# Kernel tuning notes

Measured on AMD Instinct MI355X. Metric: run time of the kernel, lower is better.

Reference implementation:

```python
import jax, jax.numpy as jnp
import numpy as np


def conv2d(x, w, groups=1, pad=0):
    # x: [N,C,H,W], w: [O, C//groups, kh, kw]
    return jax.lax.conv_general_dilated(
        x, w, window_strides=(1, 1), padding=[(pad, pad), (pad, pad)],
        dimension_numbers=("NCHW", "OIHW", "NCHW"), feature_group_count=groups)


def l2norm(x, eps=1e-12):
    # torch F.normalize over last dim: x / max(||x||_2, eps)
    n = jnp.sqrt(jnp.sum(x * x, axis=-1, keepdims=True))
    return x / jnp.maximum(n, eps)


def setup_inputs() -> dict:
    key = jax.random.key(0)
    dim, heads, b, H, W = 48, 8, 2, 256, 256
    ks = jax.random.split(key, 20)
    rn = lambda k, shp, s: (jax.random.normal(k, shp, dtype=jnp.float32) * s)
    return {
        "x1": rn(ks[0], (b, dim, H, W), 1.0),
        "x2": rn(ks[1], (b, dim, H, W), 1.0),
        "t1": jnp.ones((heads, 1, 1), jnp.float32),
        "t2": jnp.ones((heads, 1, 1), jnp.float32),
        "qkv1_w": rn(ks[2], (dim * 3, dim, 1, 1), 0.05),
        "qkv1_dw": rn(ks[3], (dim * 3, 1, 3, 3), 0.05),
        "qkv2_w": rn(ks[4], (dim * 3, dim, 1, 1), 0.05),
        "qkv2_dw": rn(ks[5], (dim * 3, 1, 3, 3), 0.05),
        "mid1_w": rn(ks[6], (dim, dim, 1, 1), 0.05),
        "mid2_w": rn(ks[7], (dim, dim, 1, 1), 0.05),
        "pE_w": rn(ks[8], (dim * 8, dim * 2, 1, 1), 0.05),
        "pE_dw": rn(ks[9], (dim * 8, 1, 3, 3), 0.05),
        "pE1_w": rn(ks[10], (dim * 4, dim, 1, 1), 0.05),
        "pE1_dw": rn(ks[11], (dim * 4, 1, 3, 3), 0.05),
        "pE2_w": rn(ks[12], (dim * 4, dim, 1, 1), 0.05),
        "pE2_dw": rn(ks[13], (dim * 4, 1, 3, 3), 0.05),
        "po1_w": rn(ks[14], (dim * 2, dim * 4, 1, 1), 0.05),
        "po2_w": rn(ks[15], (dim * 2, dim * 4, 1, 1), 0.05),
    }


def reference(x1, x2, t1, t2, qkv1_w, qkv1_dw, qkv2_w, qkv2_dw,
              mid1_w, mid2_w, pE_w, pE_dw, pE1_w, pE1_dw,
              pE2_w, pE2_dw, po1_w, po2_w):
    b, c, h, w = x1.shape
    heads = t1.shape[0]
    ch = c // heads  # channels per head

    def to_heads(t):  # [b, c, h, w] -> [b, heads, ch, h*w]
        return t.reshape(b, heads, ch, h * w)

    qkv1 = conv2d(conv2d(x1, qkv1_w), qkv1_dw, groups=3 * c, pad=1)
    q1, k1, v1 = jnp.split(qkv1, 3, axis=1)
    qkv2 = conv2d(conv2d(x2, qkv2_w), qkv2_dw, groups=3 * c, pad=1)
    q2, k2, v2 = jnp.split(qkv2, 3, axis=1)

    q1, k1, v1 = to_heads(q1), to_heads(k1), to_heads(v1)
    q2, k2, v2 = to_heads(q2), to_heads(k2), to_heads(v2)
    q1, k1 = l2norm(q1), l2norm(k1)
    q2, k2 = l2norm(q2), l2norm(k2)

    # channel cross-attention: [b, heads, ch, ch]
    attn1 = jnp.einsum("bhcn,bhdn->bhcd", q2, k1) * t1
    attn2 = jnp.einsum("bhcn,bhdn->bhcd", q1, k2) * t2
    out1 = jnp.einsum("bhcd,bhdn->bhcn", jax.nn.softmax(attn1, axis=-1), v1)
    out2 = jnp.einsum("bhcd,bhdn->bhcn", jax.nn.softmax(attn2, axis=-1), v2)
    out1 = out1.reshape(b, c, h, w)
    out2 = out2.reshape(b, c, h, w)

    x1 = x1 + conv2d(out1, mid1_w)
    x2 = x2 + conv2d(out2, mid2_w)
    out = jnp.concatenate([x1, x2], axis=1)  # [b, 2c, h, w]

    g = conv2d(conv2d(out, pE_w), pE_dw, groups=8 * c, pad=1)  # [b, 8c, h, w]
    g1, g2 = jnp.split(g, 2, axis=1)
    x1 = jax.nn.gelu(g1, approximate=False) * conv2d(conv2d(x1, pE1_w), pE1_dw, groups=4 * c, pad=1)
    x2 = jax.nn.gelu(g2, approximate=False) * conv2d(conv2d(x2, pE2_w), pE2_dw, groups=4 * c, pad=1)

    return out + conv2d(x1, po1_w) + conv2d(x2, po2_w)
```

## Files before the change

### kernel.cpp

```cpp
#include <hip/hip_runtime.h>
#include <math.h>

#define HW_ 65536

typedef __attribute__((ext_vector_type(8))) short b16x8;
typedef __attribute__((ext_vector_type(4))) short b16x4;
typedef __attribute__((ext_vector_type(4))) float f32x4;
typedef __attribute__((ext_vector_type(2))) float f32x2;

__device__ __forceinline__ unsigned short f2b(float f) {
    union { float f; unsigned u; } v; v.f = f;
    unsigned r = v.u + 0x7fffu + ((v.u >> 16) & 1u);
    return (unsigned short)(r >> 16);
}
__device__ __forceinline__ float b2f(unsigned short h) {
    union { unsigned u; float f; } v; v.u = ((unsigned)h) << 16; return v.f;
}
__device__ __forceinline__ float gelu_f(float x) {
    float t = 0.7978845608f * fmaf(0.044715f * x, x * x, x);
    float e = __expf(2.f * t);
    float th = 1.f - 2.f / (e + 1.f);
    return 0.5f * x * (1.f + th);
}

__device__ __forceinline__ f32x2 pk_fma(f32x2 a, f32x2 b, f32x2 c) {
#if __has_builtin(__builtin_elementwise_fma)
    return __builtin_elementwise_fma(a, b, c);
#else
    f32x2 r; r[0] = fmaf(a[0], b[0], c[0]); r[1] = fmaf(a[1], b[1], c[1]);
    return r;
#endif
}

__device__ __forceinline__ float wave_reduce_sum(float v) {
    #pragma unroll
    for (int off = 32; off; off >>= 1) v += __shfl_down(v, off, 64);
    return v;
}

__device__ __forceinline__ size_t baddr(long px, int CC, int g) {
    return (((size_t)(px >> 4)) * CC + g) * 128 + ((size_t)(px & 15) << 3);
}

__global__ __launch_bounds__(256) void wprep_k(
    const float* __restrict__ q1w, const float* __restrict__ q2w,
    const float* __restrict__ m1w, const float* __restrict__ m2w,
    const float* __restrict__ pEw, const float* __restrict__ p1w,
    const float* __restrict__ p2w, const float* __restrict__ o1w,
    const float* __restrict__ o2w,
    const float* __restrict__ q1dw, const float* __restrict__ q2dw,
    const float* __restrict__ pEdw, const float* __restrict__ p1dw,
    const float* __restrict__ p2dw,
    unsigned short* __restrict__ wt, float* __restrict__ dwt)
{
    const int idx = blockIdx.x * 256 + threadIdx.x;
    if (idx < 135168) {
        const int base[8] = {0,9216,18432,21504,24576,61440,98304,116736};
        int s = 0;
        #pragma unroll
        for (int i = 1; i < 8; i++) if (idx >= base[i]) s = i;
        const int local = idx - base[s];
        float v = 0.f;
        if (s < 4) {
            const int m = local >> 6, k = local & 63;
            const float* src = (s == 0) ? q1w : (s == 1) ? q2w : (s == 2) ? m1w : m2w;
            if (k < 48) v = src[m * 48 + k];
        } else if (s < 6) {
            const int br = s - 4;
            const int m = local / 96, k = local % 96;
            if (m < 192) {
                v = pEw[(size_t)(br * 192 + m) * 96 + k];
            } else {
                const float* p12 = br ? p2w : p1w;
                const int lo = br * 48, m2 = m - 192;
                if (k >= lo && k < lo + 48) v = p12[m2 * 48 + (k - lo)];
            }
        } else {
            const int m = local / 192, k = local % 192;
            v = ((s == 6) ? o1w : o2w)[m * 192 + k];
        }
        wt[idx] = f2b(v);
    } else if (idx < 135168 + 9504) {
        const int d = idx - 135168;
        const int dbase[5] = {0,1296,2592,6048,7776};
        const int Cs[5] = {144,144,384,192,192};
        int s = 0;
        #pragma unroll
        for (int i = 1; i < 5; i++) if (d >= dbase[i]) s = i;
        const int local = d - dbase[s], C = Cs[s];
        const int t = local / C, c = local % C;
        const float* src = (s == 0) ? q1dw : (s == 1) ? q2dw : (s == 2) ? pEdw
                         : (s == 3) ? p1dw : p2dw;
        dwt[d] = src[c * 9 + t];
    }
}

template<int BM, int KC, int NT, int BSRC, int EPI, int GRIDMODE>
__global__ __launch_bounds__(256) void gemm_k(
    const unsigned short* __restrict__ B16,
    const float* __restrict__ Bf32, int Cin,
    const unsigned short* __restrict__ W16,
    unsigned short* __restrict__ out16, int CCo, int Coff,
    float* __restrict__ outf, const unsigned short* __restrict__ res,
    const unsigned short* __restrict__ acc16,
    const float* __restrict__ Bf32b, const unsigned short* __restrict__ W16b,
    unsigned short* __restrict__ out16b)
{
    constexpr int MF = BM / 16;
    const int tid = threadIdx.x;
    const int lane = tid & 63, w = tid >> 6;
    const int lm = lane & 15, lk = lane >> 4;

    int mb, pxblk;
    if (GRIDMODE == 2) {
        const int bx = blockIdx.x;
        const int sb = (bx & 7) * 512 + (bx >> 3);
        mb = sb & 3; pxblk = sb >> 2;
    } else {
        mb = blockIdx.y; pxblk = blockIdx.x;
    }

    const float* Bf = Bf32;
    const unsigned short* Wp = W16;
    unsigned short* outp = out16;
    if (GRIDMODE == 0 && BSRC == 1 && blockIdx.z) {
        Bf = Bf32b; Wp = W16b; outp = out16b;
    }

    const int m0 = mb * BM;
    const long wavepx = ((long)pxblk * 4 + w) * (NT * 16);
    const long pxb0 = wavepx >> 4;

    f32x4 acc[NT][MF];
    #pragma unroll
    for (int nt = 0; nt < NT; nt++)
        #pragma unroll
        for (int m = 0; m < MF; m++)
            #pragma unroll
            for (int j = 0; j < 4; j++) acc[nt][m][j] = 0.f;

    #pragma unroll
    for (int kc = 0; kc < KC; kc++) {
        b16x8 a[MF];
        #pragma unroll
        for (int m = 0; m < MF; m++)
            a[m] = *(const b16x8*)&Wp[(size_t)(m0 + m * 16 + lm) * (KC * 32) + kc * 32 + lk * 8];
        #pragma unroll
        for (int nt = 0; nt < NT; nt++) {
            b16x8 bb;
            if (BSRC == 0) {
                bb = *(const b16x8*)&B16[((pxb0 + nt) * (KC * 4) + (kc * 4 + lk)) * 128 + lm * 8];
            } else {
                const long px = wavepx + nt * 16 + lm;
                const int p = (int)(px & 65535), bat = (int)(px >> 16);
                #pragma unroll
                for (int j = 0; j < 8; j++) {
                    const int c = kc * 32 + lk * 8 + j;
                    float v = (c < Cin) ? Bf[((size_t)(bat * Cin + c) << 16) + p] : 0.f;
                    bb[j] = (short)f2b(v);
                }
            }
            #pragma unroll
            for (int m = 0; m < MF; m++)
                acc[nt][m] = __builtin_amdgcn_mfma_f32_16x16x32_bf16(a[m], bb, acc[nt][m], 0, 0, 0);
        }
    }

    #pragma unroll
    for (int nt = 0; nt < NT; nt++) {
        const long px = wavepx + nt * 16 + lm;
        #pragma unroll
        for (int m = 0; m < MF; m++) {
            const int mrow = m * 16 + lk * 4;
            if (EPI == 0) {
                b16x4 o;
                #pragma unroll
                for (int j = 0; j < 4; j++) o[j] = (short)f2b(acc[nt][m][j]);
                const int ch = Coff + m0 + mrow;
                *(b16x4*)&outp[((pxb0 + nt) * CCo + (ch >> 3)) * 128 + lm * 8 + (ch & 7)] = o;
            } else if (EPI == 1) {
                const int p = (int)(px & 65535), bat = (int)(px >> 16);
                b16x4 r4 = *(const b16x4*)&res[((pxb0 + nt) * 12 + (mrow >> 3)) * 128 + lm * 8 + (mrow & 7)];
                #pragma unroll
                for (int j = 0; j < 4; j++)
                    outf[((size_t)(bat * 96 + mrow + j) << 16) + p]
                        = acc[nt][m][j] + b2f((unsigned short)r4[j]);
            } else if (EPI == 2) {
                const int p = (int)(px & 65535), bat = (int)(px >> 16);
                #pragma unroll
                for (int j = 0; j < 4; j++) {
                    const size_t adr = ((size_t)(bat * 96 + mrow + j) << 16) + p;
                    outf[adr] += acc[nt][m][j];
                }
            } else {
                const int p = (int)(px & 65535), bat = (int)(px >> 16);
                const size_t boffi = ((pxb0 + nt) * 12 + (mrow >> 3)) * 128 + lm * 8 + (mrow & 7);
                b16x4 r4 = *(const b16x4*)&res[boffi];
                b16x4 a4 = *(const b16x4*)&acc16[boffi];
                #pragma unroll
                for (int j = 0; j < 4; j++)
                    outf[((size_t)(bat * 96 + mrow + j) << 16) + p]
                        = acc[nt][m][j] + b2f((unsigned short)r4[j]) + b2f((unsigned short)a4[j]);
            }
        }
    }
}

__device__ __forceinline__ void unpack8v(const uint4 u, f32x2 f[4]) {
    union { unsigned u; float f; } a, b;
    a.u = u.x << 16; b.u = u.x & 0xFFFF0000u; f[0][0] = a.f; f[0][1] = b.f;
    a.u = u.y << 16; b.u = u.y & 0xFFFF0000u; f[1][0] = a.f; f[1][1] = b.f;
    a.u = u.z << 16; b.u = u.z & 0xFFFF0000u; f[2][0] = a.f; f[2][1] = b.f;
    a.u = u.w << 16; b.u = u.w & 0xFFFF0000u; f[3][0] = a.f; f[3][1] = b.f;
}

__device__ __forceinline__ void dw_row4(
    f32x2 acc[4][4], const unsigned short* __restrict__ T,
    size_t cb, long lOff, long rOff, bool lval, bool rval,
    const float* __restrict__ wrow, int wstr)
{
    f32x2 w[3][4];
    #pragma unroll
    for (int tx = 0; tx < 3; tx++) {
        const float4 a = *(const float4*)(wrow + (size_t)tx * wstr);
        const float4 b = *(const float4*)(wrow + (size_t)tx * wstr + 4);
        w[tx][0][0] = a.x; w[tx][0][1] = a.y;
        w[tx][1][0] = a.z; w[tx][1][1] = a.w;
        w[tx][2][0] = b.x; w[tx][2][1] = b.y;
        w[tx][3][0] = b.z; w[tx][3][1] = b.w;
    }
    uint4 u[6];
    if (lval) u[0] = *(const uint4*)&T[cb + lOff];
    else      u[0] = make_uint4(0u, 0u, 0u, 0u);
    #pragma unroll
    for (int c = 0; c < 4; c++) u[c + 1] = *(const uint4*)&T[cb + (size_t)c * 8];
    if (rval) u[5] = *(const uint4*)&T[cb + rOff];
    else      u[5] = make_uint4(0u, 0u, 0u, 0u);

    #pragma unroll
    for (int d = 0; d < 6; d++) {
        f32x2 f[4];
        unpack8v(u[d], f);
        #pragma unroll
        for (int tx = 0; tx < 3; tx++) {
            const int p = d - tx;
            if (p >= 0 && p < 4)
                #pragma unroll
                for (int q = 0; q < 4; q++)
                    acc[p][q] = pk_fma(w[tx][q], f[q], acc[p][q]);
        }
    }
}

__device__ __forceinline__ void dw_row2(
    f32x2 acc[2][4], const unsigned short* __restrict__ T,
    size_t cb, long lOff, long rOff, bool lval, bool rval,
    const float* __restrict__ wrow, int wstr)
{
    f32x2 w[3][4];
    #pragma unroll
    for (int tx = 0; tx < 3; tx++) {
        const float4 a = *(const float4*)(wrow + (size_t)tx * wstr);
        const float4 b = *(const float4*)(wrow + (size_t)tx * wstr + 4);
        w[tx][0][0] = a.x; w[tx][0][1] = a.y;
        w[tx][1][0] = a.z; w[tx][1][1] = a.w;
        w[tx][2][0] = b.x; w[tx][2][1] = b.y;
        w[tx][3][0] = b.z; w[tx][3][1] = b.w;
    }
    uint4 u[4];
    if (lval) u[0] = *(const uint4*)&T[cb + lOff];
    else      u[0] = make_uint4(0u, 0u, 0u, 0u);
    u[1] = *(const uint4*)&T[cb];
    u[2] = *(const uint4*)&T[cb + 8];
    if (rval) u[3] = *(const uint4*)&T[cb + rOff];
    else      u[3] = make_uint4(0u, 0u, 0u, 0u);

    #pragma unroll
    for (int c = 0; c < 4; c++) {
        f32x2 f[4];
        unpack8v(u[c], f);
        #pragma unroll
        for (int tx = 0; tx < 3; tx++) {
            const int p = c - tx;
            if (p >= 0 && p < 2)
                #pragma unroll
                for (int q = 0; q < 4; q++)
                    acc[p][q] = pk_fma(w[tx][q], f[q], acc[p][q]);
        }
    }
}

__global__ __launch_bounds__(256) void dw144_k(
    const unsigned short* __restrict__ in1, unsigned short* __restrict__ out1,
    const unsigned short* __restrict__ in2, unsigned short* __restrict__ out2,
    const float* __restrict__ dwt)
{
    const int z = blockIdx.z;
    const unsigned short* in = z ? in2 : in1;
    unsigned short* out = z ? out2 : out1;
    const float* wt = dwt + z * 1296;
    const int bx = blockIdx.x;
    const int sb = (bx & 7) * 288 + (bx >> 3);
    const int idx = sb * 256 + threadIdx.x;
    const int pbi = idx / 72;
    const int rem = idx - pbi * 72;
    const int g = rem >> 2, i = rem & 3;
    const long px0 = (long)pbi * 16 + i * 4;
    const int x0 = (int)(px0 & 255);
    const int y = (int)((px0 >> 8) & 255);
    const bool lval = x0 > 0, rval = x0 < 252;
    const int off = (int)(px0 & 15) * 8;
    const size_t cb0 = ((size_t)(px0 >> 4) * 18 + g) * 128 + off;
    const long lOff = (off == 0) ? (120 - 18 * 128) : -8;
    const long rOff = (off == 96) ? (18 * 128 - 96) : 32;
    const long dyStep = 16 * 18 * 128;

    f32x2 acc[4][4];
    #pragma unroll
    for (int p = 0; p < 4; p++)
        #pragma unroll
        for (int q = 0; q < 4; q++) { acc[p][q][0] = 0.f; acc[p][q][1] = 0.f; }

    #pragma unroll
    for (int dy = -1; dy <= 1; dy++) {
        const int yy = y + dy;
        if ((unsigned)yy >= 256u) continue;
        const size_t cb = cb0 + (size_t)((long)dy * dyStep);
        dw_row4(acc, in, cb, lOff, rOff, lval, rval,
                wt + g * 8 + (size_t)(dy + 1) * 3 * 144, 144);
    }

    #pragma unroll
    for (int p = 0; p < 4; p++) {
        b16x8 o;
        #pragma unroll
        for (int j = 0; j < 8; j++) o[j] = (short)f2b(acc[p][j >> 1][j & 1]);
        *(b16x8*)&out[cb0 + (size_t)p * 8] = o;
    }
}

__global__ __launch_bounds__(256) void dwtail_k(
    const unsigned short* __restrict__ GH, unsigned short* __restrict__ Xg,
    const float* __restrict__ dwtG, const float* __restrict__ dwtH)
{
    const int bx = blockIdx.x;
    const int sb = (bx & 7) * 768 + (bx >> 3);
    const int idx = sb * 256 + threadIdx.x;
    const int pbi = idx / 192;
    const int rem = idx - pbi * 192;
    const int g = rem >> 3, i = rem & 7;
    const long px0 = (long)pbi * 16 + i * 2;
    const int x0 = (int)(px0 & 255);
    const int y = (int)((px0 >> 8) & 255);
    const bool lval = x0 > 0, rval = x0 < 254;
    const int off = (int)(px0 & 15) * 8;
    const size_t cb0 = ((size_t)(px0 >> 4) * 48 + g) * 128 + off;
    const long lOff = (off == 0) ? (120 - 48 * 128) : -8;
    const long rOff = (off == 112) ? (48 * 128 - 112) : 16;
    const long dyStep = 16 * 48 * 128;

    f32x2 aG[2][4], aH[2][4];
    #pragma unroll
    for (int p = 0; p < 2; p++)
        #pragma unroll
        for (int q = 0; q < 4; q++) {
            aG[p][q][0] = 0.f; aG[p][q][1] = 0.f;
            aH[p][q][0] = 0.f; aH[p][q][1] = 0.f;
        }

    #pragma unroll
    for (int dy = -1; dy <= 1; dy++) {
        const int yy = y + dy;
        if ((unsigned)yy >= 256u) continue;
        const size_t cb = cb0 + (size_t)((long)dy * dyStep);
        dw_row2(aG, GH, cb, lOff, rOff, lval, rval,
                dwtG + g * 8 + (size_t)(dy + 1) * 3 * 384, 384);
        dw_row2(aH, GH, cb + 3072, lOff, rOff, lval, rval,
                dwtH + g * 8 + (size_t)(dy + 1) * 3 * 192, 192);
    }

    const size_t ob = ((size_t)(px0 >> 4) * 24 + g) * 128 + off;
    #pragma unroll
    for (int p = 0; p < 2; p++) {
        b16x8 o;
        #pragma unroll
        for (int j = 0; j < 8; j++)
            o[j] = (short)f2b(gelu_f(aG[p][j >> 1][j & 1]) * aH[p][j >> 1][j & 1]);
        *(b16x8*)&Xg[ob + (size_t)p * 8] = o;
    }
}

__global__ __launch_bounds__(256) void attnA_k(
    const unsigned short* __restrict__ Q1, const unsigned short* __restrict__ Q2,
    float* __restrict__ part)
{
    const int tid = threadIdx.x;
    const int chunk = blockIdx.x, bh = blockIdx.y, a = blockIdx.z;
    const int b = bh >> 3, h = bh & 7;
    const unsigned* Qq = (const unsigned*)(a ? Q1 : Q2);
    const unsigned* Qk = (const unsigned*)(a ? Q2 : Q1);
    const int u0 = h * 3;
    const int cq = u0 >> 2, o = u0 & 3;
    const int ck = (24 + u0) >> 2;

    float dot[36], nq[6], nk[6];
    #pragma unroll
    for (int i = 0; i < 36; i++) dot[i] = 0.f;
    #pragma unroll
    for (int i = 0; i < 6; i++) { nq[i] = 0.f; nk[i] = 0.f; }

    #pragma unroll 1
    for (int r = 0; r < 8; r++) {
        const long px = (long)b * 65536 + chunk * 2048 + r * 256 + tid;
        const size_t rowu = ((size_t)(px >> 4)) * 18 * 64 + ((px & 15) << 2);
        const uint4 qa = *(const uint4*)&Qq[rowu + (size_t)cq * 64];
        const uint4 qb = *(const uint4*)&Qq[rowu + (size_t)(cq + 1) * 64];
        const uint4 ka = *(const uint4*)&Qk[rowu + (size_t)ck * 64];
        const uint4 kb = *(const uint4*)&Qk[rowu + (size_t)(ck + 1) * 64];
        unsigned uq[3], uk[3];
        if (o == 0)      { uq[0]=qa.x; uq[1]=qa.y; uq[2]=qa.z; uk[0]=ka.x; uk[1]=ka.y; uk[2]=ka.z; }
        else if (o == 1) { uq[0]=qa.y; uq[1]=qa.z; uq[2]=qa.w; uk[0]=ka.y; uk[1]=ka.z; uk[2]=ka.w; }
        else if (o == 2) { uq[0]=qa.z; uq[1]=qa.w; uq[2]=qb.x; uk[0]=ka.z; uk[1]=ka.w; uk[2]=kb.x; }
        else             { uq[0]=qa.w; uq[1]=qb.x; uq[2]=qb.y; uk[0]=ka.w; uk[1]=kb.x; uk[2]=kb.y; }
        float q[6], k[6];
        #pragma unroll
        for (int i = 0; i < 3; i++) {
            union { unsigned u; float f; } lo, hi;
            lo.u = uq[i] << 16; hi.u = uq[i] & 0xFFFF0000u;
            q[2 * i] = lo.f; q[2 * i + 1] = hi.f;
            lo.u = uk[i] << 16; hi.u = uk[i] & 0xFFFF0000u;
            k[2 * i] = lo.f; k[2 * i + 1] = hi.f;
        }
        #pragma unroll
        for (int c = 0; c < 6; c++) nq[c] = fmaf(q[c], q[c], nq[c]);
        #pragma unroll
        for (int d = 0; d < 6; d++) nk[d] = fmaf(k[d], k[d], nk[d]);
        #pragma unroll
        for (int c = 0; c < 6; c++)
            #pragma unroll
            for (int d = 0; d < 6; d++) dot[c * 6 + d] = fmaf(q[c], k[d], dot[c * 6 + d]);
    }

    __shared__ float red[4][48];
    const int lane = tid & 63, wid = tid >> 6;
    #pragma unroll
    for (int i = 0; i < 48; i++) {
        float v = (i < 36) ? dot[i] : (i < 42 ? nq[i - 36] : nk[i - 42]);
        v = wave_reduce_sum(v);
        if (!lane) red[wid][i] = v;
    }
    __syncthreads();
    if (tid < 48)
        part[((size_t)((a * 16 + bh) * 32 + chunk)) * 48 + tid]
            = red[0][tid] + red[1][tid] + red[2][tid] + red[3][tid];
}

__global__ void attnB_k(const float* __restrict__ part,
                        const float* __restrict__ t1, const float* __restrict__ t2,
                        float* __restrict__ att)
{
    const int abh = blockIdx.x, tid = threadIdx.x;
    const int a = abh >> 4, b = (abh >> 3) & 1, h = abh & 7;
    __shared__ float s[48];
    if (tid < 48) {
        float v = 0.f;
        for (int ch = 0; ch < 32; ch++) v += part[((size_t)abh * 32 + ch) * 48 + tid];
        s[tid] = v;
    }
    __syncthreads();
    if (tid < 6) {
        const int c = tid;
        const float tv = a ? t2[h] : t1[h];
        const float qn = fmaxf(sqrtf(s[36 + c]), 1e-12f);
        float raw[6];
        #pragma unroll
        for (int d = 0; d < 6; d++)
            raw[d] = tv * s[c * 6 + d] / (qn * fmaxf(sqrtf(s[42 + d]), 1e-12f));
        float m = raw[0];
        #pragma unroll
        for (int d = 1; d < 6; d++) m = fmaxf(m, raw[d]);
        float e[6], sum = 0.f;
        #pragma unroll
        for (int d = 0; d < 6; d++) { e[d] = expf(raw[d] - m); sum += e[d]; }
        const float inv = 1.f / sum;
        #pragma unroll
        for (int d = 0; d < 6; d++)
            att[((size_t)(a * 2 + b) * 8 + h) * 36 + c * 6 + d] = e[d] * inv;
    }
}

__global__ __launch_bounds__(256) void mid_k(
    const unsigned short* __restrict__ Q1, const unsigned short* __restrict__ Q2,
    const float* __restrict__ att,
    const float* __restrict__ x1, const float* __restrict__ x2,
    const unsigned short* __restrict__ Wm, unsigned short* __restrict__ D16p)
{
    const int br = blockIdx.y;
    const unsigned short* Qv = br ? Q2 : Q1;
    const float* x = br ? x2 : x1;
    const unsigned short* W16 = Wm + br * 3072;
    const float* attb = att + br * 576;
    const int boff = br * 48;

    __shared__ float atts[288];
    __shared__ unsigned short S[256][72];
    const int tid = threadIdx.x;
    const long px = (long)blockIdx.x * 256 + tid;
    const int bat = (int)(px >> 16);

    for (int i = tid; i < 288; i += 256) atts[i] = attb[bat * 288 + i];

    float v[48];
    #pragma unroll
    for (int i = 0; i < 6; i++) {
        b16x8 t = *(const b16x8*)&Qv[baddr(px, 18, 12 + i)];
        #pragma unroll
        for (int j = 0; j < 8; j++) v[i * 8 + j] = b2f((unsigned short)t[j]);
    }
    __syncthreads();

    #pragma unroll
    for (int h = 0; h < 8; h++) {
        unsigned short sh[6];
        #pragma unroll
        for (int c = 0; c < 6; c++) {
            float s = 0.f;
            #pragma unroll
            for (int d = 0; d < 6; d++) s = fmaf(atts[h * 36 + c * 6 + d], v[h * 6 + d], s);
            sh[c] = f2b(s);
        }
        #pragma unroll
        for (int i = 0; i < 3; i++) {
            unsigned packed = (unsigned)sh[2 * i] | ((unsigned)sh[2 * i + 1] << 16);
            *(unsigned*)&S[tid][h * 6 + 2 * i] = packed;
        }
    }
    #pragma unroll
    for (int i = 0; i < 8; i++) *(unsigned*)&S[tid][48 + 2 * i] = 0u;
    __syncthreads();

    const int lane = tid & 63, w = tid >> 6;
    const int lm = lane & 15, lk = lane >> 4;
    f32x4 acc[4][3];
    #pragma unroll
    for (int nt = 0; nt < 4; nt++)
        #pragma unroll
        for (int m = 0; m < 3; m++)
            #pragma unroll
            for (int j = 0; j < 4; j++) acc[nt][m][j] = 0.f;

    #pragma unroll
    for (int kc = 0; kc < 2; kc++) {
        b16x8 a[3];
        #pragma unroll
        for (int m = 0; m < 3; m++)
            a[m] = *(const b16x8*)&W16[(size_t)(m * 16 + lm) * 64 + kc * 32 + lk * 8];
        #pragma unroll
        for (int nt = 0; nt < 4; nt++) {
            b16x8 bb = *(const b16x8*)&S[w * 64 + nt * 16 + lm][kc * 32 + lk * 8];
            #pragma unroll
            for (int m = 0; m < 3; m++)
                acc[nt][m] = __builtin_amdgcn_mfma_f32_16x16x32_bf16(a[m], bb, acc[nt][m], 0, 0, 0);
        }
    }

    #pragma unroll
    for (int nt = 0; nt < 4; nt++) {
        const long px2 = (long)blockIdx.x * 256 + w * 64 + nt * 16 + lm;
        const int p2 = (int)(px2 & 65535);
        const long pxb2 = px2 >> 4;
        #pragma unroll
        for (int m = 0; m < 3; m++) {
            const int row = m * 16 + lk * 4;
            b16x4 o;
            #pragma unroll
            for (int j = 0; j < 4; j++) {
                float xv = x[((size_t)(bat * 48 + row + j) << 16) + p2];
                o[j] = (short)f2b(acc[nt][m][j] + xv);
            }
            const int ch = boff + row;
            *(b16x4*)&D16p[(pxb2 * 12 + (ch >> 3)) * 128 + lm * 8 + (ch & 7)] = o;
        }
    }
}

extern "C" void kernel_launch(void* const* d_in, const int* in_sizes, int n_in,
                              void* d_out, int out_size, void* d_ws, size_t ws_size,
                              hipStream_t stream) {
    const float* x1      = (const float*)d_in[0];
    const float* x2      = (const float*)d_in[1];
    const float* t1      = (const float*)d_in[2];
    const float* t2      = (const float*)d_in[3];
    const float* qkv1_w  = (const float*)d_in[4];
    const float* qkv1_dw = (const float*)d_in[5];
    const float* qkv2_w  = (const float*)d_in[6];
    const float* qkv2_dw = (const float*)d_in[7];
    const float* mid1_w  = (const float*)d_in[8];
    const float* mid2_w  = (const float*)d_in[9];
    const float* pE_w    = (const float*)d_in[10];
    const float* pE_dw   = (const float*)d_in[11];
    const float* pE1_w   = (const float*)d_in[12];
    const float* pE1_dw  = (const float*)d_in[13];
    const float* pE2_w   = (const float*)d_in[14];
    const float* pE2_dw  = (const float*)d_in[15];
    const float* po1_w   = (const float*)d_in[16];
    const float* po2_w   = (const float*)d_in[17];
    float* dout = (float*)d_out;
    char* ws = (char*)d_ws;

    unsigned short* D16p  = (unsigned short*)(ws + 0);
    unsigned short* QKVc1 = (unsigned short*)(ws + 25165824);
    unsigned short* QKVc2 = (unsigned short*)(ws + 62914560);
    unsigned short* Q1    = (unsigned short*)(ws + 100663296);
    unsigned short* Q2    = (unsigned short*)(ws + 138412032);
    unsigned short* GH    = (unsigned short*)(ws + 25165824);
    unsigned short* Xg    = (unsigned short*)(ws + 125829120);
    float*          PART  = (float*)(ws + 176160768);
    float*          ATT   = (float*)(ws + 176357376);
    unsigned short* W16   = (unsigned short*)(ws + 176361984);
    float*          DWT   = (float*)(ws + 176632320);
    unsigned short* ACC   = (unsigned short*)(ws + 176670720);

    const dim3 blk(256);

    wprep_k<<<dim3(566), blk, 0, stream>>>(
        qkv1_w, qkv2_w, mid1_w, mid2_w, pE_w, pE1_w, pE2_w, po1_w, po2_w,
        qkv1_dw, qkv2_dw, pE_dw, pE1_dw, pE2_dw, W16, DWT);

    gemm_k<144,2,2,1,0,0><<<dim3(1024,1,2), blk, 0, stream>>>(
        nullptr, x1, 48, W16, QKVc1, 18, 0, nullptr, nullptr, nullptr,
        x2, W16 + 9216, QKVc2);
    dw144_k<<<dim3(2304,1,2), blk, 0, stream>>>(QKVc1, Q1, QKVc2, Q2, DWT);

    attnA_k<<<dim3(32,16,2), blk, 0, stream>>>(Q1, Q2, PART);
    attnB_k<<<dim3(32), dim3(64), 0, stream>>>(PART, t1, t2, ATT);

    mid_k<<<dim3(512,2), blk, 0, stream>>>(Q1, Q2, ATT, x1, x2, W16 + 18432, D16p);

    for (int br = 0; br < 2; br++) {
        gemm_k<96,3,2,0,0,2><<<dim3(4096), blk, 0, stream>>>(
            D16p, nullptr, 0, W16 + 24576 + br * 36864, GH, 48, 0,
            nullptr, nullptr, nullptr, nullptr, nullptr, nullptr);
        dwtail_k<<<dim3(6144), blk, 0, stream>>>(
            GH, Xg, DWT + 2592 + br * 192, DWT + (br ? 7776 : 6048));
        if (br == 0)
            gemm_k<96,6,2,0,0,0><<<dim3(1024,1), blk, 0, stream>>>(
                Xg, nullptr, 0, W16 + 98304, ACC, 12, 0, nullptr, nullptr, nullptr,
                nullptr, nullptr, nullptr);
        else
            gemm_k<96,6,2,0,3,0><<<dim3(1024,1), blk, 0, stream>>>(
                Xg, nullptr, 0, W16 + 116736, nullptr, 0, 0, dout, D16p, ACC,
                nullptr, nullptr, nullptr);
    }
}
```

Baseline: 378.0 us.

## Fuse both output projections into one K-split GEMM and halve dw144 per-thread work

Both gated branches now write separate Xg buffers, and a single GEMM with K=384 reads the first half of K from Xg1 and the second half from Xg2. This replaces two po GEMMs and the bf16 ACC round trip, so the intermediate partial sum is no longer written, reread or rounded to bf16. The dw144 kernel also processes 2 pixels per thread instead of 4, doubling the grid to raise occupancy, at the cost of more redundant halo loads. The extra workspace for Xg2 pushes the buffers to larger offsets.

```diff
diff --git a/kernel.cpp b/kernel.cpp
--- a/kernel.cpp
+++ b/kernel.cpp
@@ -55,7 +55,7 @@
 {
     const int idx = blockIdx.x * 256 + threadIdx.x;
     if (idx < 135168) {
-        const int base[8] = {0,9216,18432,21504,24576,61440,98304,116736};
+        const int base[8] = {0,9216,18432,21504,24576,61440,98304,135168};
         int s = 0;
         #pragma unroll
         for (int i = 1; i < 8; i++) if (idx >= base[i]) s = i;
@@ -76,8 +76,8 @@
                 if (k >= lo && k < lo + 48) v = p12[m2 * 48 + (k - lo)];
             }
         } else {
-            const int m = local / 192, k = local % 192;
-            v = ((s == 6) ? o1w : o2w)[m * 192 + k];
+            const int m = local / 384, k = local % 384;
+            v = (k < 192) ? o1w[m * 192 + k] : o2w[m * 192 + (k - 192)];
         }
         wt[idx] = f2b(v);
     } else if (idx < 135168 + 9504) {
@@ -95,7 +95,7 @@
     }
 }
 
-template<int BM, int KC, int NT, int BSRC, int EPI, int GRIDMODE>
+template<int BM, int KC, int NT, int BSRC, int EPI, int GRIDMODE, bool KSPLIT = false>
 __global__ __launch_bounds__(256) void gemm_k(
     const unsigned short* __restrict__ B16,
     const float* __restrict__ Bf32, int Cin,
@@ -149,7 +149,13 @@
         for (int nt = 0; nt < NT; nt++) {
             b16x8 bb;
             if (BSRC == 0) {
-                bb = *(const b16x8*)&B16[((pxb0 + nt) * (KC * 4) + (kc * 4 + lk)) * 128 + lm * 8];
+                if (KSPLIT) {
+                    const unsigned short* Bs = (kc >= KC / 2) ? acc16 : B16;
+                    const int kc2 = (kc >= KC / 2) ? kc - KC / 2 : kc;
+                    bb = *(const b16x8*)&Bs[((pxb0 + nt) * ((KC / 2) * 4) + (kc2 * 4 + lk)) * 128 + lm * 8];
+                } else {
+                    bb = *(const b16x8*)&B16[((pxb0 + nt) * (KC * 4) + (kc * 4 + lk)) * 128 + lm * 8];
+                }
             } else {
                 const long px = wavepx + nt * 16 + lm;
                 const int p = (int)(px & 65535), bat = (int)(px >> 16);
@@ -192,15 +198,6 @@
                     const size_t adr = ((size_t)(bat * 96 + mrow + j) << 16) + p;
                     outf[adr] += acc[nt][m][j];
                 }
-            } else {
-                const int p = (int)(px & 65535), bat = (int)(px >> 16);
-                const size_t boffi = ((pxb0 + nt) * 12 + (mrow >> 3)) * 128 + lm * 8 + (mrow & 7);
-                b16x4 r4 = *(const b16x4*)&res[boffi];
-                b16x4 a4 = *(const b16x4*)&acc16[boffi];
-                #pragma unroll
-                for (int j = 0; j < 4; j++)
-                    outf[((size_t)(bat * 96 + mrow + j) << 16) + p]
-                        = acc[nt][m][j] + b2f((unsigned short)r4[j]) + b2f((unsigned short)a4[j]);
             }
         }
     }
@@ -214,8 +211,8 @@
     a.u = u.w << 16; b.u = u.w & 0xFFFF0000u; f[3][0] = a.f; f[3][1] = b.f;
 }
 
-__device__ __forceinline__ void dw_row4(
-    f32x2 acc[4][4], const unsigned short* __restrict__ T,
+__device__ __forceinline__ void dw_row2(
+    f32x2 acc[2][4], const unsigned short* __restrict__ T,
     size_t cb, long lOff, long rOff, bool lval, bool rval,
     const float* __restrict__ wrow, int wstr)
 {
@@ -229,44 +226,6 @@
         w[tx][2][0] = b.x; w[tx][2][1] = b.y;
         w[tx][3][0] = b.z; w[tx][3][1] = b.w;
     }
-    uint4 u[6];
-    if (lval) u[0] = *(const uint4*)&T[cb + lOff];
-    else      u[0] = make_uint4(0u, 0u, 0u, 0u);
-    #pragma unroll
-    for (int c = 0; c < 4; c++) u[c + 1] = *(const uint4*)&T[cb + (size_t)c * 8];
-    if (rval) u[5] = *(const uint4*)&T[cb + rOff];
-    else      u[5] = make_uint4(0u, 0u, 0u, 0u);
-
-    #pragma unroll
-    for (int d = 0; d < 6; d++) {
-        f32x2 f[4];
-        unpack8v(u[d], f);
-        #pragma unroll
-        for (int tx = 0; tx < 3; tx++) {
-            const int p = d - tx;
-            if (p >= 0 && p < 4)
-                #pragma unroll
-                for (int q = 0; q < 4; q++)
-                    acc[p][q] = pk_fma(w[tx][q], f[q], acc[p][q]);
-        }
-    }
-}
-
-__device__ __forceinline__ void dw_row2(
-    f32x2 acc[2][4], const unsigned short* __restrict__ T,
-    size_t cb, long lOff, long rOff, bool lval, bool rval,
-    const float* __restrict__ wrow, int wstr)
-{
-    f32x2 w[3][4];
-    #pragma unroll
-    for (int tx = 0; tx < 3; tx++) {
-        const float4 a = *(const float4*)(wrow + (size_t)tx * wstr);
-        const float4 b = *(const float4*)(wrow + (size_t)tx * wstr + 4);
-        w[tx][0][0] = a.x; w[tx][0][1] = a.y;
-        w[tx][1][0] = a.z; w[tx][1][1] = a.w;
-        w[tx][2][0] = b.x; w[tx][2][1] = b.y;
-        w[tx][3][0] = b.z; w[tx][3][1] = b.w;
-    }
     uint4 u[4];
     if (lval) u[0] = *(const uint4*)&T[cb + lOff];
     else      u[0] = make_uint4(0u, 0u, 0u, 0u);
@@ -300,24 +259,24 @@
     unsigned short* out = z ? out2 : out1;
     const float* wt = dwt + z * 1296;
     const int bx = blockIdx.x;
-    const int sb = (bx & 7) * 288 + (bx >> 3);
+    const int sb = (bx & 7) * 576 + (bx >> 3);
     const int idx = sb * 256 + threadIdx.x;
-    const int pbi = idx / 72;
-    const int rem = idx - pbi * 72;
-    const int g = rem >> 2, i = rem & 3;
-    const long px0 = (long)pbi * 16 + i * 4;
+    const int pbi = idx / 144;
+    const int rem = idx - pbi * 144;
+    const int g = rem >> 3, i = rem & 7;
+    const long px0 = (long)pbi * 16 + i * 2;
     const int x0 = (int)(px0 & 255);
     const int y = (int)((px0 >> 8) & 255);
-    const bool lval = x0 > 0, rval = x0 < 252;
+    const bool lval = x0 > 0, rval = x0 < 254;
     const int off = (int)(px0 & 15) * 8;
     const size_t cb0 = ((size_t)(px0 >> 4) * 18 + g) * 128 + off;
     const long lOff = (off == 0) ? (120 - 18 * 128) : -8;
-    const long rOff = (off == 96) ? (18 * 128 - 96) : 32;
+    const long rOff = (off == 112) ? (18 * 128 - 112) : 16;
     const long dyStep = 16 * 18 * 128;
 
-    f32x2 acc[4][4];
-    #pragma unroll
-    for (int p = 0; p < 4; p++)
+    f32x2 acc[2][4];
+    #pragma unroll
+    for (int p = 0; p < 2; p++)
         #pragma unroll
         for (int q = 0; q < 4; q++) { acc[p][q][0] = 0.f; acc[p][q][1] = 0.f; }
 
@@ -326,12 +285,12 @@
         const int yy = y + dy;
         if ((unsigned)yy >= 256u) continue;
         const size_t cb = cb0 + (size_t)((long)dy * dyStep);
-        dw_row4(acc, in, cb, lOff, rOff, lval, rval,
+        dw_row2(acc, in, cb, lOff, rOff, lval, rval,
                 wt + g * 8 + (size_t)(dy + 1) * 3 * 144, 144);
     }
 
     #pragma unroll
-    for (int p = 0; p < 4; p++) {
+    for (int p = 0; p < 2; p++) {
         b16x8 o;
         #pragma unroll
         for (int j = 0; j < 8; j++) o[j] = (short)f2b(acc[p][j >> 1][j & 1]);
@@ -614,12 +573,12 @@
     unsigned short* Q1    = (unsigned short*)(ws + 100663296);
     unsigned short* Q2    = (unsigned short*)(ws + 138412032);
     unsigned short* GH    = (unsigned short*)(ws + 25165824);
-    unsigned short* Xg    = (unsigned short*)(ws + 125829120);
-    float*          PART  = (float*)(ws + 176160768);
-    float*          ATT   = (float*)(ws + 176357376);
-    unsigned short* W16   = (unsigned short*)(ws + 176361984);
-    float*          DWT   = (float*)(ws + 176632320);
-    unsigned short* ACC   = (unsigned short*)(ws + 176670720);
+    unsigned short* Xg1   = (unsigned short*)(ws + 125829120);
+    unsigned short* Xg2   = (unsigned short*)(ws + 176160768);
+    unsigned short* W16   = (unsigned short*)(ws + 226492416);
+    float*          DWT   = (float*)(ws + 226762752);
+    float*          PART  = (float*)(ws + 226800768);
+    float*          ATT   = (float*)(ws + 226997376);
 
     const dim3 blk(256);
 
@@ -630,7 +589,7 @@
     gemm_k<144,2,2,1,0,0><<<dim3(1024,1,2), blk, 0, stream>>>(
         nullptr, x1, 48, W16, QKVc1, 18, 0, nullptr, nullptr, nullptr,
         x2, W16 + 9216, QKVc2);
-    dw144_k<<<dim3(2304,1,2), blk, 0, stream>>>(QKVc1, Q1, QKVc2, Q2, DWT);
+    dw144_k<<<dim3(4608,1,2), blk, 0, stream>>>(QKVc1, Q1, QKVc2, Q2, DWT);
 
     attnA_k<<<dim3(32,16,2), blk, 0, stream>>>(Q1, Q2, PART);
     attnB_k<<<dim3(32), dim3(64), 0, stream>>>(PART, t1, t2, ATT);
@@ -642,14 +601,10 @@
             D16p, nullptr, 0, W16 + 24576 + br * 36864, GH, 48, 0,
             nullptr, nullptr, nullptr, nullptr, nullptr, nullptr);
         dwtail_k<<<dim3(6144), blk, 0, stream>>>(
-            GH, Xg, DWT + 2592 + br * 192, DWT + (br ? 7776 : 6048));
-        if (br == 0)
-            gemm_k<96,6,2,0,0,0><<<dim3(1024,1), blk, 0, stream>>>(
-                Xg, nullptr, 0, W16 + 98304, ACC, 12, 0, nullptr, nullptr, nullptr,
-                nullptr, nullptr, nullptr);
-        else
-            gemm_k<96,6,2,0,3,0><<<dim3(1024,1), blk, 0, stream>>>(
-                Xg, nullptr, 0, W16 + 116736, nullptr, 0, 0, dout, D16p, ACC,
-                nullptr, nullptr, nullptr);
-    }
-}
+            GH, br ? Xg2 : Xg1, DWT + 2592 + br * 192, DWT + (br ? 7776 : 6048));
+    }
+
+    gemm_k<96,12,2,0,1,0,true><<<dim3(1024,1), blk, 0, stream>>>(
+        Xg1, nullptr, 0, W16 + 98304, nullptr, 0, 0, dout, D16p, Xg2,
+        nullptr, nullptr, nullptr);
+}
```

Result: faster. 354.1 us (-6.3%).
